# Performance work log

Hardware: AMD Instinct MI355X
Metric: run time of the kernel (lower is better)

Reference implementation:

```python
import jax, jax.numpy as jnp
import numpy as np

B, S, HID = 4, 2048, 2048
NH, NKV, D = 16, 8, 128
RK, RV = 16, 16
HPG = NH // NKV
SCALING = D ** -0.5
NEG = -1e9


def _rope(x, cos, sin):
    # x: [B, S, H, D]; cos/sin: [S, D//2]. Gemma split-half complex rotation.
    x1, x2 = jnp.split(x, 2, axis=-1)
    c = cos[None, :, None, :]
    s = sin[None, :, None, :]
    return jnp.concatenate([x1 * c - x2 * s, x1 * s + x2 * c], axis=-1)


def setup_inputs() -> dict:
    key = jax.random.key(0)
    ks = jax.random.split(key, 8)
    hidden_states = jax.random.normal(ks[0], (B, S, HID), dtype=jnp.float32)
    # RoPE frequencies (theta=10000)
    inv_freq = 1.0 / (10000.0 ** (np.arange(0, D, 2, dtype=np.float32) / D))
    ang = np.arange(S, dtype=np.float32)[:, None] * inv_freq[None, :]
    freqs_cos = jnp.asarray(np.cos(ang), dtype=jnp.float32)
    freqs_sin = jnp.asarray(np.sin(ang), dtype=jnp.float32)
    kv_write_indices = jnp.arange(S, dtype=jnp.int32)
    # causal additive mask [1,1,S,S]
    causal = jnp.tril(jnp.ones((S, S), dtype=bool))
    mask = jnp.where(causal, 0.0, NEG).astype(jnp.float32)[None, None]
    sc = 0.02
    W_q = jax.random.normal(ks[1], (NH * D, HID), dtype=jnp.float32) * sc
    W_k = jax.random.normal(ks[2], (NKV * D, HID), dtype=jnp.float32) * sc
    W_v = jax.random.normal(ks[3], (NKV * D, HID), dtype=jnp.float32) * sc
    o_proj_w = jax.random.normal(ks[4], (HID, NH * D), dtype=jnp.float32) * sc
    V_r_basis = jax.random.normal(ks[5], (NH, D, RK), dtype=jnp.float32) * (D ** -0.5)
    Z_v_basis = jax.random.normal(ks[6], (NKV, D, RV), dtype=jnp.float32) * (D ** -0.5)
    return {"hidden_states": hidden_states, "freqs_cos": freqs_cos, "freqs_sin": freqs_sin,
            "kv_write_indices": kv_write_indices, "mask": mask, "W_q": W_q, "W_k": W_k,
            "W_v": W_v, "o_proj_w": o_proj_w, "V_r_basis": V_r_basis, "Z_v_basis": Z_v_basis}


def reference(hidden_states, freqs_cos, freqs_sin, kv_write_indices, mask,
              W_q, W_k, W_v, o_proj_w, V_r_basis, Z_v_basis):
    bsz, q_len, _ = hidden_states.shape
    q = (hidden_states @ W_q.T).reshape(bsz, q_len, NH, D)
    k = (hidden_states @ W_k.T).reshape(bsz, q_len, NKV, D)
    v = (hidden_states @ W_v.T).reshape(bsz, q_len, NKV, D)

    # project K per-head onto its group's basis (vectorized over the head loop)
    head_to_group = jnp.arange(NH) // HPG                       # [NH]
    k_per_head = k[:, :, head_to_group, :]                      # [B,S,NH,D]
    pk = jnp.einsum('bshd,hdr->bshr', k_per_head, V_r_basis)    # [B,S,NH,RK]
    pv = jnp.einsum('bqgd,gdr->bqgr', v, Z_v_basis)             # [B,S,NKV,RV]

    # factorized cache write (scatter along seq dim), prefill: kv_seq_len = S
    kv_seq_len = q_len
    cache_pk = jnp.zeros((bsz, kv_seq_len, NH, RK), hidden_states.dtype)
    cache_pv = jnp.zeros((bsz, kv_seq_len, NKV, RV), hidden_states.dtype)
    cache_pk = cache_pk.at[:, kv_write_indices].set(pk)
    cache_pv = cache_pv.at[:, kv_write_indices].set(pv)

    # reconstruct K/V from compressed cache
    k_hat = jnp.einsum('bshr,hrd->bshd', cache_pk, jnp.swapaxes(V_r_basis, -1, -2))
    v_hat = jnp.einsum('bsgr,grd->bsgd', cache_pv, jnp.swapaxes(Z_v_basis, -1, -2))

    # RoPE post-reconstruction
    q_rot = _rope(q, freqs_cos[:q_len], freqs_sin[:q_len])
    k_rot = _rope(k_hat, freqs_cos[:kv_seq_len], freqs_sin[:kv_seq_len])

    # GQA: repeat kv heads
    v_g = jnp.repeat(v_hat, HPG, axis=2)                        # [B,S,NH,D]

    scores = jnp.einsum('bqhd,bkhd->bhqk', q_rot, k_rot) * SCALING
    scores = scores + mask[:, :, :q_len, :kv_seq_len]
    probs = jax.nn.softmax(scores.astype(jnp.float32), axis=-1).astype(hidden_states.dtype)
    out = jnp.einsum('bhqk,bkhd->bqhd', probs, v_g)
    out = out.reshape(bsz, q_len, NH * D)
    return out @ o_proj_w.T
```

## Files before the change

kernel.cpp:

```cpp
#include <hip/hip_runtime.h>

typedef unsigned short ushort8 __attribute__((ext_vector_type(8)));
typedef short s16x8 __attribute__((ext_vector_type(8)));
typedef float f32x4 __attribute__((ext_vector_type(4)));

#define AS1 __attribute__((address_space(1)))
#define AS3 __attribute__((address_space(3)))

#define B_    4
#define S_    2048
#define HID_  2048
#define NH_   16
#define NKV_  8
#define D_    128
#define RK_   16
#define SCALING_ 0.08838834764831845f
#define LOG2E_   1.4426950408889634f
#define NEGBIG   -1.0e30f

__device__ __forceinline__ float bf2f(unsigned short u) {
  union { unsigned int i; float f; } x; x.i = ((unsigned int)u) << 16; return x.f;
}
__device__ __forceinline__ unsigned short f2bf(float f) {
  union { float f; unsigned int i; } x; x.f = f;
  unsigned int r = x.i + 0x7fffu + ((x.i >> 16) & 1u);
  return (unsigned short)(r >> 16);
}

__global__ __launch_bounds__(256) void cvt_bf16(const float* __restrict__ in,
                                                unsigned short* __restrict__ out,
                                                int n8) {
  int i = blockIdx.x * 256 + threadIdx.x;
  const int stride = gridDim.x * 256;
  for (; i < n8; i += stride) {
    const float4 a = ((const float4*)in)[i * 2];
    const float4 b = ((const float4*)in)[i * 2 + 1];
    ushort8 u;
    u[0] = f2bf(a.x); u[1] = f2bf(a.y); u[2] = f2bf(a.z); u[3] = f2bf(a.w);
    u[4] = f2bf(b.x); u[5] = f2bf(b.y); u[6] = f2bf(b.z); u[7] = f2bf(b.w);
    *(ushort8*)&out[i * 8] = u;
  }
}

__global__ __launch_bounds__(256) void wfuse(const float* __restrict__ W_k,
                                             const float* __restrict__ W_v,
                                             const float* __restrict__ Vr,
                                             const float* __restrict__ Zv,
                                             unsigned short* __restrict__ Wf) {
  const int idx = blockIdx.x;
  const int cc = blockIdx.y * 256;
  const int tid = threadIdx.x;
  const bool isK = idx < 16;
  const int hg = isK ? idx : (idx - 16);
  const int wrow0 = isK ? (idx * 16) : (256 + (idx - 16) * 16);
  const float* W = isK ? &W_k[(size_t)((hg >> 1) * 128) * HID_]
                       : &W_v[(size_t)(hg * 128) * HID_];
  const float* P = isK ? &Vr[(size_t)hg * 128 * 16] : &Zv[(size_t)hg * 128 * 16];
  __shared__ float Wl[32][257];
  float acc[16] = {};
  for (int d0 = 0; d0 < 128; d0 += 32) {
    __syncthreads();
#pragma unroll 8
    for (int dd = 0; dd < 32; ++dd)
      Wl[dd][tid] = W[(size_t)(d0 + dd) * HID_ + cc + tid];
    __syncthreads();
#pragma unroll 8
    for (int dd = 0; dd < 32; ++dd) {
      const float w = Wl[dd][tid];
#pragma unroll
      for (int r = 0; r < 16; ++r) acc[r] += w * P[(d0 + dd) * 16 + r];
    }
  }
#pragma unroll
  for (int r = 0; r < 16; ++r)
    Wf[(size_t)(wrow0 + r) * HID_ + cc + tid] = f2bf(acc[r]);
}

template<bool CBF>
__global__ __launch_bounds__(256) void gemm_mfma(const unsigned short* __restrict__ A,
                                                 const unsigned short* __restrict__ Bb,
                                                 void* __restrict__ C_,
                                                 int M, int N, int K) {
  __shared__ unsigned short Ash[128 * 64];
  __shared__ unsigned short Bsh[128 * 64];
  const int tid = threadIdx.x;
  const int w = tid >> 6, l = tid & 63, lg = l >> 4, ll = l & 15;
  const int wr = w >> 1, wc = w & 1;
  const int flat = blockIdx.y * gridDim.x + blockIdx.x;
  const int cpx = (gridDim.x * gridDim.y) >> 3;
  const int swz = (flat & 7) * cpx + (flat >> 3);
  const int bm = (swz / gridDim.x) * 128, bn = (swz % gridDim.x) * 128;

  f32x4 acc[4][4];
#pragma unroll
  for (int i = 0; i < 4; i++)
#pragma unroll
    for (int j = 0; j < 4; j++) acc[i][j] = (f32x4){0.f, 0.f, 0.f, 0.f};

  const int srow = tid >> 3;
  const int sslot = tid & 7;

  for (int k0 = 0; k0 < K; k0 += 64) {
    __syncthreads();
#pragma unroll
    for (int c = 0; c < 4; ++c) {
      const int row = c * 32 + srow;
      const int ss = sslot ^ (row & 7);
      const unsigned short* srcA = &A[(size_t)(bm + row) * K + k0 + ss * 8];
      const unsigned short* srcB = &Bb[(size_t)(bn + row) * K + k0 + ss * 8];
      char* dstA = ((char*)Ash) + c * 4096 + w * 1024;
      char* dstB = ((char*)Bsh) + c * 4096 + w * 1024;
      __builtin_amdgcn_global_load_lds((const AS1 void*)srcA, (AS3 void*)dstA, 16, 0, 0);
      __builtin_amdgcn_global_load_lds((const AS1 void*)srcB, (AS3 void*)dstB, 16, 0, 0);
    }
    __syncthreads();

#pragma unroll
    for (int ks = 0; ks < 2; ++ks) {
      s16x8 af[4], bf_[4];
#pragma unroll
      for (int mi = 0; mi < 4; ++mi) {
        const int row = wr * 64 + mi * 16 + ll;
        af[mi] = *(const s16x8*)&Ash[row * 64 + (((ks * 4 + lg) ^ (row & 7)) * 8)];
      }
#pragma unroll
      for (int ni = 0; ni < 4; ++ni) {
        const int row = wc * 64 + ni * 16 + ll;
        bf_[ni] = *(const s16x8*)&Bsh[row * 64 + (((ks * 4 + lg) ^ (row & 7)) * 8)];
      }
#pragma unroll
      for (int mi = 0; mi < 4; ++mi)
#pragma unroll
        for (int ni = 0; ni < 4; ++ni)
          acc[mi][ni] = __builtin_amdgcn_mfma_f32_16x16x32_bf16(af[mi], bf_[ni], acc[mi][ni], 0, 0, 0);
    }
  }

#pragma unroll
  for (int mi = 0; mi < 4; ++mi)
#pragma unroll
    for (int ni = 0; ni < 4; ++ni)
#pragma unroll
      for (int j = 0; j < 4; ++j) {
        const int row = bm + wr * 64 + mi * 16 + lg * 4 + j;
        const int col = bn + wc * 64 + ni * 16 + ll;
        if (CBF) ((unsigned short*)C_)[(size_t)row * N + col] = f2bf(acc[mi][ni][j]);
        else     ((float*)C_)[(size_t)row * N + col] = acc[mi][ni][j];
      }
}

__global__ __launch_bounds__(256) void rope_q(unsigned short* __restrict__ q,
                                              const float* __restrict__ cosT,
                                              const float* __restrict__ sinT) {
  const int p = blockIdx.x * 256 + threadIdx.x;
  const int d = p & 63;
  const int h = (p >> 6) & 15;
  const int s = (p >> 10) & 2047;
  const int b = p >> 21;
  const size_t base = (((size_t)b * S_ + s) * NH_ + h) * D_ + d;
  const float x1 = bf2f(q[base]), x2 = bf2f(q[base + 64]);
  const float c = cosT[s * 64 + d], sn = sinT[s * 64 + d];
  const float sc = SCALING_ * LOG2E_;
  q[base]      = f2bf((x1 * c - x2 * sn) * sc);
  q[base + 64] = f2bf((x1 * sn + x2 * c) * sc);
}

__global__ __launch_bounds__(256) void expand_k(const float* __restrict__ pkpv,
                                                const float* __restrict__ Vr,
                                                const float* __restrict__ cosT,
                                                const float* __restrict__ sinT,
                                                unsigned short* __restrict__ kr) {
  const int s0 = blockIdx.x * 32, h = blockIdx.y, b = blockIdx.z;
  const int tid = threadIdx.x;
  __shared__ float pkS[32][17];
  if (tid < 128) {
    const int r_ = tid >> 2, c4 = (tid & 3) * 4;
    float4 v = *(const float4*)&pkpv[(size_t)(b * S_ + s0 + r_) * 384 + h * 16 + c4];
    pkS[r_][c4 + 0] = v.x; pkS[r_][c4 + 1] = v.y;
    pkS[r_][c4 + 2] = v.z; pkS[r_][c4 + 3] = v.w;
  }
  __syncthreads();
  const int row = tid >> 3, dl = tid & 7;
  float kh[16];
#pragma unroll
  for (int j = 0; j < 16; j++) {
    const int d = dl + 8 * j;
    const float4* w = (const float4*)&Vr[((size_t)h * D_ + d) * RK_];
    float a = 0.f;
#pragma unroll
    for (int q4 = 0; q4 < 4; q4++) {
      float4 wv = w[q4];
      a += pkS[row][q4 * 4 + 0] * wv.x + pkS[row][q4 * 4 + 1] * wv.y
         + pkS[row][q4 * 4 + 2] * wv.z + pkS[row][q4 * 4 + 3] * wv.w;
    }
    kh[j] = a;
  }
  const int pos = s0 + row;
  const size_t o = (((size_t)b * NH_ + h) * S_ + pos) * D_;
#pragma unroll
  for (int j = 0; j < 8; j++) {
    const int d = dl + 8 * j;
    const float c = cosT[pos * 64 + d], sn = sinT[pos * 64 + d];
    kr[o + d]      = f2bf(kh[j] * c - kh[j + 8] * sn);
    kr[o + d + 64] = f2bf(kh[j] * sn + kh[j + 8] * c);
  }
}

__global__ __launch_bounds__(256) void expand_v(const float* __restrict__ pkpv,
                                                const float* __restrict__ Zv,
                                                unsigned short* __restrict__ vh) {
  const int s0 = blockIdx.x * 32, g = blockIdx.y, b = blockIdx.z;
  const int tid = threadIdx.x;
  __shared__ float pvS[32][17];
  if (tid < 128) {
    const int r_ = tid >> 2, c4 = (tid & 3) * 4;
    float4 v = *(const float4*)&pkpv[(size_t)(b * S_ + s0 + r_) * 384 + 256 + g * 16 + c4];
    pvS[r_][c4 + 0] = v.x; pvS[r_][c4 + 1] = v.y;
    pvS[r_][c4 + 2] = v.z; pvS[r_][c4 + 3] = v.w;
  }
  __syncthreads();
  const int row = tid >> 3, dl = tid & 7;
  const size_t o = (((size_t)b * NKV_ + g) * S_ + s0 + row) * D_;
#pragma unroll
  for (int j = 0; j < 16; j++) {
    const int d = dl + 8 * j;
    const float4* w = (const float4*)&Zv[((size_t)g * D_ + d) * RK_];
    float a = 0.f;
#pragma unroll
    for (int q4 = 0; q4 < 4; q4++) {
      float4 wv = w[q4];
      a += pvS[row][q4 * 4 + 0] * wv.x + pvS[row][q4 * 4 + 1] * wv.y
         + pvS[row][q4 * 4 + 2] * wv.z + pvS[row][q4 * 4 + 3] * wv.w;
    }
    vh[o + d] = f2bf(a);
  }
}

__global__ __launch_bounds__(256) void attn_mfma(const unsigned short* __restrict__ q,
                                                 const unsigned short* __restrict__ kr,
                                                 const unsigned short* __restrict__ vh,
                                                 unsigned short* __restrict__ out) {
  const int flat = ((int)blockIdx.z * 16 + (int)blockIdx.y) * 16 + (int)blockIdx.x;
  const int swz = (flat & 7) * 128 + (flat >> 3);
  const int qt = 15 - (swz & 15);
  const int h = (swz >> 4) & 15;
  const int b = swz >> 8;
  const int g = h >> 1;
  const int tid = threadIdx.x;
  const int w = tid >> 6, l = tid & 63, lg = l >> 4, ll = l & 15;

  __shared__ unsigned short Klds[2][64 * 128];
  __shared__ unsigned short Vt[2][128 * 64];
  __shared__ unsigned short Ps[4][32 * 64];

  const int qr0 = qt * 128 + w * 32;
  const int ktmax = 2 * qt + 1;
  const int kmy = 2 * qt + (w >> 1);

  s16x8 qf[2][4];
#pragma unroll
  for (int mi = 0; mi < 2; ++mi)
#pragma unroll
    for (int ks = 0; ks < 4; ++ks)
      qf[mi][ks] = *(const s16x8*)&q[(((size_t)b * S_ + qr0 + mi * 16 + ll) * NH_ + h) * D_ + ks * 32 + lg * 8];

  f32x4 o[2][8];
#pragma unroll
  for (int mi = 0; mi < 2; ++mi)
#pragma unroll
    for (int nd = 0; nd < 8; ++nd) o[mi][nd] = (f32x4){0.f, 0.f, 0.f, 0.f};
  float m_[2][4], l_[2][4];
#pragma unroll
  for (int mi = 0; mi < 2; ++mi)
#pragma unroll
    for (int j = 0; j < 4; ++j) { m_[mi][j] = NEGBIG; l_[mi][j] = 0.f; }

  const unsigned short* kbase = &kr[(((size_t)b * NH_ + h) * S_) * D_];
  const unsigned short* vbase = &vh[(((size_t)b * NKV_ + g) * S_) * D_];
  const int vk = (tid & 31) * 2, d0v = (tid >> 5) * 16;

  ushort8 va0, va1, vb0, vb1;
  {
#pragma unroll
    for (int c = 0; c < 4; ++c) {
      const int ro = c * 16 + w * 4 + lg;
      const int ss = ll ^ (ro & 7);
      const unsigned short* src = kbase + ro * D_ + ss * 8;
      char* dst = ((char*)&Klds[0][0]) + c * 4096 + w * 1024;
      __builtin_amdgcn_global_load_lds((const AS1 void*)src, (AS3 void*)dst, 16, 0, 0);
    }
    const unsigned short* v0 = vbase + (size_t)vk * D_ + d0v;
    va0 = *(const ushort8*)v0; va1 = *(const ushort8*)(v0 + 8);
    vb0 = *(const ushort8*)(v0 + D_); vb1 = *(const ushort8*)(v0 + D_ + 8);
#pragma unroll
    for (int j = 0; j < 8; ++j) {
      const int d1 = d0v + j, d2 = d0v + 8 + j;
      *(unsigned int*)&Vt[0][d1 * 64 + (((vk >> 3) ^ (d1 & 7)) * 8) + (vk & 7)] =
          (unsigned int)va0[j] | ((unsigned int)vb0[j] << 16);
      *(unsigned int*)&Vt[0][d2 * 64 + (((vk >> 3) ^ (d2 & 7)) * 8) + (vk & 7)] =
          (unsigned int)va1[j] | ((unsigned int)vb1[j] << 16);
    }
  }
  __syncthreads();

  for (int kt = 0; kt <= ktmax; ++kt) {
    const int p = kt & 1;
    if (kt < ktmax) {
      const unsigned short* kb2 = kbase + (size_t)(kt + 1) * 64 * D_;
#pragma unroll
      for (int c = 0; c < 4; ++c) {
        const int ro = c * 16 + w * 4 + lg;
        const int ss = ll ^ (ro & 7);
        const unsigned short* src = kb2 + ro * D_ + ss * 8;
        char* dst = ((char*)&Klds[p ^ 1][0]) + c * 4096 + w * 1024;
        __builtin_amdgcn_global_load_lds((const AS1 void*)src, (AS3 void*)dst, 16, 0, 0);
      }
      const unsigned short* v0 = vbase + (size_t)((kt + 1) * 64 + vk) * D_ + d0v;
      va0 = *(const ushort8*)v0; va1 = *(const ushort8*)(v0 + 8);
      vb0 = *(const ushort8*)(v0 + D_); vb1 = *(const ushort8*)(v0 + D_ + 8);
    }

    if (kt <= kmy) {
      f32x4 s[2][4];
#pragma unroll
      for (int mi = 0; mi < 2; ++mi)
#pragma unroll
        for (int ni = 0; ni < 4; ++ni) s[mi][ni] = (f32x4){0.f, 0.f, 0.f, 0.f};
#pragma unroll
      for (int ks = 0; ks < 4; ++ks) {
#pragma unroll
        for (int ni = 0; ni < 4; ++ni) {
          const int row = ni * 16 + ll;
          const s16x8 kf = *(const s16x8*)&Klds[p][row * 128 + (((ks * 4 + lg) ^ (row & 7)) * 8)];
          s[0][ni] = __builtin_amdgcn_mfma_f32_16x16x32_bf16(qf[0][ks], kf, s[0][ni], 0, 0, 0);
          s[1][ni] = __builtin_amdgcn_mfma_f32_16x16x32_bf16(qf[1][ks], kf, s[1][ni], 0, 0, 0);
        }
      }

      const bool diag = (kt == kmy);
      float lm[2][4];
#pragma unroll
      for (int mi = 0; mi < 2; ++mi)
#pragma unroll
        for (int j = 0; j < 4; ++j) {
          if (diag) {
            const int qg = qr0 + mi * 16 + lg * 4 + j;
#pragma unroll
            for (int ni = 0; ni < 4; ++ni)
              if (kt * 64 + ni * 16 + ll > qg) s[mi][ni][j] = NEGBIG;
          }
          lm[mi][j] = fmaxf(fmaxf(s[mi][0][j], s[mi][1][j]),
                            fmaxf(s[mi][2][j], s[mi][3][j]));
        }
      float excess = lm[0][0] - m_[0][0];
#pragma unroll
      for (int mi = 0; mi < 2; ++mi)
#pragma unroll
        for (int j = 0; j < 4; ++j) excess = fmaxf(excess, lm[mi][j] - m_[mi][j]);
      const bool slow = __any(excess > 11.5f);

#pragma unroll
      for (int mi = 0; mi < 2; ++mi)
#pragma unroll
        for (int j = 0; j < 4; ++j) {
          float ps_[4];
          if (slow) {
            float mt = lm[mi][j];
            mt = fmaxf(mt, __shfl_xor(mt, 1));
            mt = fmaxf(mt, __shfl_xor(mt, 2));
            mt = fmaxf(mt, __shfl_xor(mt, 4));
            mt = fmaxf(mt, __shfl_xor(mt, 8));
            const float mnew = fmaxf(m_[mi][j], mt);
            const float al = exp2f(m_[mi][j] - mnew);
            m_[mi][j] = mnew;
            float sum = 0.f;
#pragma unroll
            for (int ni = 0; ni < 4; ++ni) { ps_[ni] = exp2f(s[mi][ni][j] - mnew); sum += ps_[ni]; }
            l_[mi][j] = l_[mi][j] * al + sum;
#pragma unroll
            for (int nd = 0; nd < 8; ++nd) o[mi][nd][j] *= al;
          } else {
            float sum = 0.f;
#pragma unroll
            for (int ni = 0; ni < 4; ++ni) { ps_[ni] = exp2f(s[mi][ni][j] - m_[mi][j]); sum += ps_[ni]; }
            l_[mi][j] += sum;
          }
          const int prow = mi * 16 + lg * 4 + j;
#pragma unroll
          for (int nq = 0; nq < 2; ++nq) {
            unsigned int u;
            asm("v_cvt_pk_bf16_f32 %0, %1, %2" : "=v"(u) : "v"(ps_[nq * 2]), "v"(ps_[nq * 2 + 1]));
            const int c0 = nq * 32 + ll, c1 = nq * 32 + 16 + ll;
            Ps[w][prow * 64 + (((c0 >> 3) ^ (prow & 7)) * 8) + (ll & 7)] = (unsigned short)u;
            Ps[w][prow * 64 + (((c1 >> 3) ^ (prow & 7)) * 8) + (ll & 7)] = (unsigned short)(u >> 16);
          }
        }

      s16x8 pa[2][2];
#pragma unroll
      for (int mi = 0; mi < 2; ++mi)
#pragma unroll
        for (int ks2 = 0; ks2 < 2; ++ks2) {
          const int prow = mi * 16 + ll;
          pa[mi][ks2] = *(const s16x8*)&Ps[w][prow * 64 + (((ks2 * 4 + lg) ^ (prow & 7)) * 8)];
        }
#pragma unroll
      for (int nd = 0; nd < 8; ++nd) {
#pragma unroll
        for (int ks2 = 0; ks2 < 2; ++ks2) {
          const int vr = nd * 16 + ll;
          const s16x8 vbf = *(const s16x8*)&Vt[p][vr * 64 + (((ks2 * 4 + lg) ^ (vr & 7)) * 8)];
          o[0][nd] = __builtin_amdgcn_mfma_f32_16x16x32_bf16(pa[0][ks2], vbf, o[0][nd], 0, 0, 0);
          o[1][nd] = __builtin_amdgcn_mfma_f32_16x16x32_bf16(pa[1][ks2], vbf, o[1][nd], 0, 0, 0);
        }
      }
    }

    if (kt < ktmax) {
#pragma unroll
      for (int j = 0; j < 8; ++j) {
        const int d1 = d0v + j, d2 = d0v + 8 + j;
        *(unsigned int*)&Vt[p ^ 1][d1 * 64 + (((vk >> 3) ^ (d1 & 7)) * 8) + (vk & 7)] =
            (unsigned int)va0[j] | ((unsigned int)vb0[j] << 16);
        *(unsigned int*)&Vt[p ^ 1][d2 * 64 + (((vk >> 3) ^ (d2 & 7)) * 8) + (vk & 7)] =
            (unsigned int)va1[j] | ((unsigned int)vb1[j] << 16);
      }
    }
    __syncthreads();
  }

#pragma unroll
  for (int mi = 0; mi < 2; ++mi)
#pragma unroll
    for (int j = 0; j < 4; ++j) {
      float ls = l_[mi][j];
      ls += __shfl_xor(ls, 1);
      ls += __shfl_xor(ls, 2);
      ls += __shfl_xor(ls, 4);
      ls += __shfl_xor(ls, 8);
      const float inv = 1.f / ls;
      const size_t rowg = (size_t)b * S_ + qr0 + mi * 16 + lg * 4 + j;
      unsigned short* op = &out[rowg * (NH_ * D_) + h * D_ + ll];
#pragma unroll
      for (int nd = 0; nd < 8; ++nd) op[nd * 16] = f2bf(o[mi][nd][j] * inv);
    }
}

extern "C" void kernel_launch(void* const* d_in, const int* in_sizes, int n_in,
                              void* d_out, int out_size, void* d_ws, size_t ws_size,
                              hipStream_t stream) {
  const float* hidden = (const float*)d_in[0];
  const float* cosT   = (const float*)d_in[1];
  const float* sinT   = (const float*)d_in[2];
  const float* W_q    = (const float*)d_in[5];
  const float* W_k    = (const float*)d_in[6];
  const float* W_v    = (const float*)d_in[7];
  const float* W_o    = (const float*)d_in[8];
  const float* Vr     = (const float*)d_in[9];
  const float* Zv     = (const float*)d_in[10];
  float* out = (float*)d_out;

  char* ws = (char*)d_ws;
  unsigned short* hb     = (unsigned short*)(ws + 0);
  unsigned short* attn_b = (unsigned short*)(ws + 0);
  unsigned short* q_b    = (unsigned short*)(ws + 33554432);
  unsigned short* kr_b   = (unsigned short*)(ws + 67108864);
  unsigned short* Wf     = (unsigned short*)(ws + 100663296);
  unsigned short* vh_b   = (unsigned short*)(ws + 100663296);
  unsigned short* WR1    = (unsigned short*)(ws + 117440512);
  float*          pkpv   = (float*)(ws + 117440512);

  const int M = B_ * S_;

  cvt_bf16<<<2048, 256, 0, stream>>>(hidden, hb, (B_ * S_ * HID_) / 8);
  cvt_bf16<<<2048, 256, 0, stream>>>(W_q, WR1, (HID_ * HID_) / 8);
  gemm_mfma<true><<<dim3(16, 64), 256, 0, stream>>>(hb, WR1, q_b, M, 2048, HID_);

  wfuse<<<dim3(24, 8), 256, 0, stream>>>(W_k, W_v, Vr, Zv, Wf);
  gemm_mfma<false><<<dim3(3, 64), 256, 0, stream>>>(hb, Wf, pkpv, M, 384, HID_);

  rope_q<<<(B_ * S_ * NH_ * 64) / 256, 256, 0, stream>>>(q_b, cosT, sinT);

  expand_k<<<dim3(S_ / 32, NH_, B_), 256, 0, stream>>>(pkpv, Vr, cosT, sinT, kr_b);
  expand_v<<<dim3(S_ / 32, NKV_, B_), 256, 0, stream>>>(pkpv, Zv, vh_b);

  cvt_bf16<<<2048, 256, 0, stream>>>(W_o, WR1, (HID_ * HID_) / 8);

  attn_mfma<<<dim3(16, 16, 4), 256, 0, stream>>>(q_b, kr_b, vh_b, attn_b);

  gemm_mfma<false><<<dim3(16, 64), 256, 0, stream>>>(attn_b, WR1, out, M, HID_, HID_);
}
```

Measured before the change: 752.4 us.

## Split attention KV range into two halves with a log-sum-exp combine kernel

Each query tile's causal KV range is split into two halves handled by separate blocks, doubling the attention grid from 1024 to 2048 blocks to even out the causal load imbalance and fill the GPU better. Each half writes unnormalized bf16 partial outputs plus per-row max and sum, and a new combine kernel merges them with log-sum-exp rescaling into the q buffer before the output projection. This adds extra global traffic for the partials and one more launch, and is only used when the workspace is large enough.

```diff
diff --git a/kernel.cpp b/kernel.cpp
--- a/kernel.cpp
+++ b/kernel.cpp
@@ -236,15 +236,31 @@
   }
 }
 
+template<bool SPLIT>
 __global__ __launch_bounds__(256) void attn_mfma(const unsigned short* __restrict__ q,
                                                  const unsigned short* __restrict__ kr,
                                                  const unsigned short* __restrict__ vh,
-                                                 unsigned short* __restrict__ out) {
-  const int flat = ((int)blockIdx.z * 16 + (int)blockIdx.y) * 16 + (int)blockIdx.x;
-  const int swz = (flat & 7) * 128 + (flat >> 3);
-  const int qt = 15 - (swz & 15);
-  const int h = (swz >> 4) & 15;
-  const int b = swz >> 8;
+                                                 unsigned short* __restrict__ outp,
+                                                 unsigned short* __restrict__ P0,
+                                                 unsigned short* __restrict__ P1,
+                                                 float2* __restrict__ ml0,
+                                                 float2* __restrict__ ml1) {
+  int qt, h, b, half;
+  if constexpr (SPLIT) {
+    const int flat = ((int)blockIdx.z * 16 + (int)blockIdx.y) * 32 + (int)blockIdx.x;
+    const int swz = (flat & 7) * 256 + (flat >> 3);
+    qt = 15 - (swz & 15);
+    half = (swz >> 4) & 1;
+    h = (swz >> 5) & 15;
+    b = swz >> 9;
+  } else {
+    const int flat = ((int)blockIdx.z * 16 + (int)blockIdx.y) * 16 + (int)blockIdx.x;
+    const int swz = (flat & 7) * 128 + (flat >> 3);
+    qt = 15 - (swz & 15);
+    half = 0;
+    h = (swz >> 4) & 15;
+    b = swz >> 8;
+  }
   const int g = h >> 1;
   const int tid = threadIdx.x;
   const int w = tid >> 6, l = tid & 63, lg = l >> 4, ll = l & 15;
@@ -254,7 +270,8 @@
   __shared__ unsigned short Ps[4][32 * 64];
 
   const int qr0 = qt * 128 + w * 32;
-  const int ktmax = 2 * qt + 1;
+  const int kt0   = SPLIT ? (half ? qt + 1 : 0)          : 0;
+  const int ktend = SPLIT ? (half ? 2 * qt + 1 : qt)     : 2 * qt + 1;
   const int kmy = 2 * qt + (w >> 1);
 
   s16x8 qf[2][4];
@@ -281,15 +298,16 @@
 
   ushort8 va0, va1, vb0, vb1;
   {
+    const unsigned short* kb0 = kbase + (size_t)kt0 * 64 * D_;
 #pragma unroll
     for (int c = 0; c < 4; ++c) {
       const int ro = c * 16 + w * 4 + lg;
       const int ss = ll ^ (ro & 7);
-      const unsigned short* src = kbase + ro * D_ + ss * 8;
+      const unsigned short* src = kb0 + ro * D_ + ss * 8;
       char* dst = ((char*)&Klds[0][0]) + c * 4096 + w * 1024;
       __builtin_amdgcn_global_load_lds((const AS1 void*)src, (AS3 void*)dst, 16, 0, 0);
     }
-    const unsigned short* v0 = vbase + (size_t)vk * D_ + d0v;
+    const unsigned short* v0 = vbase + (size_t)(kt0 * 64 + vk) * D_ + d0v;
     va0 = *(const ushort8*)v0; va1 = *(const ushort8*)(v0 + 8);
     vb0 = *(const ushort8*)(v0 + D_); vb1 = *(const ushort8*)(v0 + D_ + 8);
 #pragma unroll
@@ -303,9 +321,9 @@
   }
   __syncthreads();
 
-  for (int kt = 0; kt <= ktmax; ++kt) {
-    const int p = kt & 1;
-    if (kt < ktmax) {
+  for (int kt = kt0; kt <= ktend; ++kt) {
+    const int p = (kt - kt0) & 1;
+    if (kt < ktend) {
       const unsigned short* kb2 = kbase + (size_t)(kt + 1) * 64 * D_;
 #pragma unroll
       for (int c = 0; c < 4; ++c) {
@@ -416,7 +434,7 @@
       }
     }
 
-    if (kt < ktmax) {
+    if (kt < ktend) {
 #pragma unroll
       for (int j = 0; j < 8; ++j) {
         const int d1 = d0v + j, d2 = d0v + 8 + j;
@@ -438,12 +456,44 @@
       ls += __shfl_xor(ls, 2);
       ls += __shfl_xor(ls, 4);
       ls += __shfl_xor(ls, 8);
-      const float inv = 1.f / ls;
-      const size_t rowg = (size_t)b * S_ + qr0 + mi * 16 + lg * 4 + j;
-      unsigned short* op = &out[rowg * (NH_ * D_) + h * D_ + ll];
-#pragma unroll
-      for (int nd = 0; nd < 8; ++nd) op[nd * 16] = f2bf(o[mi][nd][j] * inv);
-    }
+      if constexpr (SPLIT) {
+        unsigned short* Ph = half ? P1 : P0;
+        float2* mlh = half ? ml1 : ml0;
+        const size_t ridx = ((size_t)b * NH_ + h) * S_ + qr0 + mi * 16 + lg * 4 + j;
+        unsigned short* op = &Ph[ridx * D_ + ll];
+#pragma unroll
+        for (int nd = 0; nd < 8; ++nd) op[nd * 16] = f2bf(o[mi][nd][j]);
+        if (ll == 0) mlh[ridx] = make_float2(m_[mi][j], ls);
+      } else {
+        const float inv = 1.f / ls;
+        const size_t rowg = (size_t)b * S_ + qr0 + mi * 16 + lg * 4 + j;
+        unsigned short* op = &outp[rowg * (NH_ * D_) + h * D_ + ll];
+#pragma unroll
+        for (int nd = 0; nd < 8; ++nd) op[nd * 16] = f2bf(o[mi][nd][j] * inv);
+      }
+    }
+}
+
+__global__ __launch_bounds__(256) void attn_combine(const unsigned short* __restrict__ P0,
+                                                    const unsigned short* __restrict__ P1,
+                                                    const float2* __restrict__ ml0,
+                                                    const float2* __restrict__ ml1,
+                                                    unsigned short* __restrict__ outp) {
+  const int s = blockIdx.x, b = blockIdx.y;
+  const int tid = threadIdx.x;
+  const int h = tid >> 4, d0 = (tid & 15) * 8;
+  const size_t ridx = ((size_t)b * NH_ + h) * S_ + s;
+  const float2 a = ml0[ridx], c = ml1[ridx];
+  const float m = fmaxf(a.x, c.x);
+  const float a0 = exp2f(a.x - m), a1 = exp2f(c.x - m);
+  const float inv = 1.f / (a0 * a.y + a1 * c.y);
+  const ushort8 u0 = *(const ushort8*)&P0[ridx * D_ + d0];
+  const ushort8 u1 = *(const ushort8*)&P1[ridx * D_ + d0];
+  ushort8 r;
+#pragma unroll
+  for (int j = 0; j < 8; ++j)
+    r[j] = f2bf((a0 * bf2f(u0[j]) + a1 * bf2f(u1[j])) * inv);
+  *(ushort8*)&outp[((size_t)b * S_ + s) * (NH_ * D_) + h * D_ + d0] = r;
 }
 
 extern "C" void kernel_launch(void* const* d_in, const int* in_sizes, int n_in,
@@ -463,12 +513,18 @@
   char* ws = (char*)d_ws;
   unsigned short* hb     = (unsigned short*)(ws + 0);
   unsigned short* attn_b = (unsigned short*)(ws + 0);
+  unsigned short* P0     = (unsigned short*)(ws + 0);
   unsigned short* q_b    = (unsigned short*)(ws + 33554432);
   unsigned short* kr_b   = (unsigned short*)(ws + 67108864);
   unsigned short* Wf     = (unsigned short*)(ws + 100663296);
   unsigned short* vh_b   = (unsigned short*)(ws + 100663296);
   unsigned short* WR1    = (unsigned short*)(ws + 117440512);
   float*          pkpv   = (float*)(ws + 117440512);
+  unsigned short* P1     = (unsigned short*)(ws + 130023424);
+  float2*         ml0    = (float2*)(ws + 163577856);
+  float2*         ml1    = (float2*)(ws + 164626432);
+  const size_t NEED_SPLIT = 165675008ull;
+  const bool split = (ws_size >= NEED_SPLIT);
 
   const int M = B_ * S_;
 
@@ -486,7 +542,14 @@
 
   cvt_bf16<<<2048, 256, 0, stream>>>(W_o, WR1, (HID_ * HID_) / 8);
 
-  attn_mfma<<<dim3(16, 16, 4), 256, 0, stream>>>(q_b, kr_b, vh_b, attn_b);
-
-  gemm_mfma<false><<<dim3(16, 64), 256, 0, stream>>>(attn_b, WR1, out, M, HID_, HID_);
-}
+  if (split) {
+    attn_mfma<true><<<dim3(32, 16, 4), 256, 0, stream>>>(q_b, kr_b, vh_b, nullptr,
+                                                         P0, P1, ml0, ml1);
+    attn_combine<<<dim3(S_, B_), 256, 0, stream>>>(P0, P1, ml0, ml1, q_b);
+    gemm_mfma<false><<<dim3(16, 64), 256, 0, stream>>>(q_b, WR1, out, M, HID_, HID_);
+  } else {
+    attn_mfma<false><<<dim3(16, 16, 4), 256, 0, stream>>>(q_b, kr_b, vh_b, attn_b,
+                                                          nullptr, nullptr, nullptr, nullptr);
+    gemm_mfma<false><<<dim3(16, 64), 256, 0, stream>>>(attn_b, WR1, out, M, HID_, HID_);
+  }
+}
```

New measurement: 747.0 us. No clear change (-0.7%).
